# Kernel optimization log

Measured on AMD Instinct MI355X. Metric: run time of the kernel, lower is better.

## Reference

```python
import jax, jax.numpy as jnp
import numpy as np

NUM_GRAPHS = 64


def gcn_conv(x, W, b, src, dst, deg_inv_sqrt, n_nodes):
    # x: [N, Fin] -> [N, Fout]; src/dst include self-loops
    h = x @ W                                   # [N, Fout]
    norm = deg_inv_sqrt[src] * deg_inv_sqrt[dst]  # [E+N]
    msg = h[src] * norm[:, None]                # gather + scale
    out = jax.ops.segment_sum(msg, dst, num_segments=n_nodes)  # scatter-add
    return out + b


def setup_inputs() -> dict:
    key = jax.random.key(0)
    ks = jax.random.split(key, 12)
    N, E, IND, H, OUT = 100000, 1600000, 128, 64, 2
    x = jax.random.normal(ks[0], (N, IND), dtype=jnp.float32)
    edge_index = jax.random.randint(ks[1], (2, E), 0, N, dtype=jnp.int64)
    batch = jnp.sort(jax.random.randint(ks[2], (N,), 0, NUM_GRAPHS, dtype=jnp.int64))
    def glorot(k, shape):
        lim = (6.0 / (shape[0] + shape[1])) ** 0.5
        return jax.random.uniform(k, shape, jnp.float32, -lim, lim)
    W1 = glorot(ks[3], (IND, 84)); b1 = jnp.zeros((84,), jnp.float32)
    W2 = glorot(ks[4], (84, H));   b2 = jnp.zeros((H,), jnp.float32)
    W3 = glorot(ks[5], (H, 32));   b3 = jnp.zeros((32,), jnp.float32)
    Wl = glorot(ks[6], (32, OUT)); bl = jnp.zeros((OUT,), jnp.float32)
    return {"x": x, "edge_index": edge_index, "batch": batch,
            "W1": W1, "b1": b1, "W2": W2, "b2": b2,
            "W3": W3, "b3": b3, "Wl": Wl, "bl": bl}


def reference(x, edge_index, batch, W1, b1, W2, b2, W3, b3, Wl, bl):
    n = x.shape[0]
    loops = jnp.arange(n, dtype=edge_index.dtype)
    # GCNConv adds self-loops before symmetric normalization
    src = jnp.concatenate([edge_index[0], loops])
    dst = jnp.concatenate([edge_index[1], loops])
    deg = jax.ops.segment_sum(jnp.ones_like(dst, dtype=x.dtype), dst, num_segments=n)
    dis = jnp.where(deg > 0, jax.lax.rsqrt(jnp.maximum(deg, 1.0)), 0.0)

    h = jax.nn.relu(gcn_conv(x, W1, b1, src, dst, dis, n))
    h = jax.nn.relu(gcn_conv(h, W2, b2, src, dst, dis, n))
    h = jax.nn.relu(gcn_conv(h, W3, b3, src, dst, dis, n))

    # global mean pool over graphs
    sums = jax.ops.segment_sum(h, batch, num_segments=NUM_GRAPHS)      # [G, 32]
    cnts = jax.ops.segment_sum(jnp.ones((n,), h.dtype), batch, num_segments=NUM_GRAPHS)
    pooled = sums / jnp.maximum(cnts, 1.0)[:, None]
    # dropout is identity in eval mode
    return pooled @ Wl + bl
```

## Files before the change

kernel.cpp:

```cpp
#include <hip/hip_runtime.h>
#include <hip/hip_bf16.h>

typedef __attribute__((ext_vector_type(8))) short bf16x8;
typedef __attribute__((ext_vector_type(4))) float f32x4;

__device__ inline short f2bf(float f) {
    __hip_bfloat16 h = __float2bfloat16(f);
    return *reinterpret_cast<short*>(&h);
}


__global__ void zero_k(float* __restrict__ p, int n) {
    for (int i = blockIdx.x * blockDim.x + threadIdx.x; i < n;
         i += gridDim.x * blockDim.x)
        p[i] = 0.0f;
}


__global__ __launch_bounds__(256) void bucket_hist_k(
    const int* __restrict__ dst, int* __restrict__ T, int E, int NB)
{
    __shared__ int hist[512];
    for (int b = threadIdx.x; b < NB; b += 256) hist[b] = 0;
    __syncthreads();
    int per = (E + gridDim.x - 1) / gridDim.x;
    int s = blockIdx.x * per;
    int e = min(E, s + per);
    for (int i = s + threadIdx.x; i < e; i += 256)
        atomicAdd(&hist[dst[i] >> 8], 1);
    __syncthreads();
    for (int b = threadIdx.x; b < NB; b += 256)
        T[b * gridDim.x + blockIdx.x] = hist[b];
}

__global__ __launch_bounds__(256) void scan_block_k(
    const int* __restrict__ in, int* __restrict__ out,
    int* __restrict__ bsum, int n)
{
    __shared__ int ts[256];
    int base = blockIdx.x * 2048;
    int i0 = base + threadIdx.x * 8;
    int vals[8];
    int s = 0;
#pragma unroll
    for (int j = 0; j < 8; ++j) {
        int v = (i0 + j) < n ? in[i0 + j] : 0;
        vals[j] = v; s += v;
    }
    ts[threadIdx.x] = s;
    __syncthreads();
    for (int d = 1; d < 256; d <<= 1) {
        int t = (threadIdx.x >= (unsigned)d) ? ts[threadIdx.x - d] : 0;
        __syncthreads();
        ts[threadIdx.x] += t;
        __syncthreads();
    }
    int run = ts[threadIdx.x] - s;
    if (threadIdx.x == 255) bsum[blockIdx.x] = ts[255];
#pragma unroll
    for (int j = 0; j < 8; ++j) {
        if (i0 + j < n) out[i0 + j] = run;
        run += vals[j];
    }
}

__global__ void scan_partials_k(int* __restrict__ bsum, int nb) {
    if (threadIdx.x == 0 && blockIdx.x == 0) {
        int run = 0;
        for (int i = 0; i < nb; ++i) { int t = bsum[i]; bsum[i] = run; run += t; }
    }
}

__global__ void scan_add_k(int* __restrict__ rp, const int* __restrict__ bsum,
                           int n, int E)
{
    int i = blockIdx.x * blockDim.x + threadIdx.x;
    if (i < n) rp[i] += bsum[i >> 11];
    if (i == 0) rp[n] = E;
}

__global__ __launch_bounds__(256) void bucket_scatter_k(
    const int* __restrict__ src, const int* __restrict__ dst,
    const int* __restrict__ Tsc, uint2* __restrict__ pairs, int E, int NB)
{
    __shared__ int cur[512];
    for (int b = threadIdx.x; b < NB; b += 256)
        cur[b] = Tsc[b * gridDim.x + blockIdx.x];
    __syncthreads();
    int per = (E + gridDim.x - 1) / gridDim.x;
    int s = blockIdx.x * per;
    int e = min(E, s + per);
    for (int i = s + threadIdx.x; i < e; i += 256) {
        int d = dst[i];
        int pos = atomicAdd(&cur[d >> 8], 1);
        pairs[pos] = make_uint2((unsigned)d, (unsigned)src[i]);
    }
}

__global__ __launch_bounds__(256) void bucket_csr_k(
    const uint2* __restrict__ pairs, const int* __restrict__ Tsc,
    int* __restrict__ row_ptr, float* __restrict__ dis,
    int* __restrict__ csr, int N, int E, int NB, int G)
{
    __shared__ int cnt[256];
    __shared__ int ts[256];
    __shared__ int cur[256];
    const int b = blockIdx.x;
    const int node0 = b << 8;
    const int e0 = Tsc[b * G];
    const int e1 = Tsc[(b + 1) * G];
    const int j = threadIdx.x;
    cnt[j] = 0;
    __syncthreads();
    for (int i = e0 + j; i < e1; i += 256)
        atomicAdd(&cnt[pairs[i].x & 255u], 1);
    __syncthreads();
    int c = cnt[j];
    ts[j] = c;
    __syncthreads();
    for (int d = 1; d < 256; d <<= 1) {
        int t = (j >= d) ? ts[j - d] : 0;
        __syncthreads();
        ts[j] += t;
        __syncthreads();
    }
    int excl = ts[j] - c;
    int node = node0 + j;
    if (node < N) {
        row_ptr[node] = e0 + excl;
        dis[node] = rsqrtf(1.0f + (float)c);
    }
    cur[j] = e0 + excl;
    if (b == NB - 1 && j == 0) row_ptr[N] = E;
    __syncthreads();
    for (int i = e0 + j; i < e1; i += 256) {
        uint2 p = pairs[i];
        int pos = atomicAdd(&cur[p.x & 255u], 1);
        csr[pos] = (int)p.y;
    }
}


template<int FIN, int FOUT, int NKK, int CT>
__global__ void wfrag_build_k(const float* __restrict__ W,
                              __hip_bfloat16* __restrict__ out)
{
    int idx = blockIdx.x * 256 + threadIdx.x;
    if (idx >= CT * NKK * 64 * 8) return;
    int e = idx & 7;
    int lane = (idx >> 3) & 63;
    int t = idx >> 9;
    int kk = t % NKK, nn = t / NKK;
    int col = nn * 16 + (lane & 15);
    int k = kk * 32 + (lane >> 4) * 8 + e;
    float v = (k < FIN && col < FOUT) ? W[k * FOUT + col] : 0.f;
    out[idx] = __float2bfloat16(v);
}


template<int FIN>
__device__ inline bf16x8 load_a8(const float* __restrict__ p, int k0) {
    bf16x8 r;
    if (k0 + 8 <= FIN) {
        float4 v0 = *reinterpret_cast<const float4*>(p + k0);
        float4 v1 = *reinterpret_cast<const float4*>(p + k0 + 4);
        r[0] = f2bf(v0.x); r[1] = f2bf(v0.y); r[2] = f2bf(v0.z); r[3] = f2bf(v0.w);
        r[4] = f2bf(v1.x); r[5] = f2bf(v1.y); r[6] = f2bf(v1.z); r[7] = f2bf(v1.w);
    } else {
#pragma unroll
        for (int e = 0; e < 8; ++e)
            r[e] = (k0 + e < FIN) ? f2bf(p[k0 + e]) : (short)0;
    }
    return r;
}

template<int FIN, int FOUT, int NKK, int CT>
__global__ __launch_bounds__(256) void gemm_mfma_v5(
    const float* __restrict__ in, const __hip_bfloat16* __restrict__ wfrag,
    const float* __restrict__ dis, __hip_bfloat16* __restrict__ hh, int n)
{
    const int tid = threadIdx.x;
    const long long base = (long long)blockIdx.x * 64;
    const int cnt = (int)min((long long)64, (long long)n - base);
    const int wv = tid >> 6, lane = tid & 63;
    const int rlo = lane & 15, kg = lane >> 4, kb = kg * 8;
    const int arow = wv * 16 + rlo;
    const long long row = base + arow;

    bf16x8 a[NKK];
    if (arow < cnt) {
        const float* p = &in[(size_t)row * FIN];
#pragma unroll
        for (int kk = 0; kk < NKK; ++kk)
            a[kk] = load_a8<FIN>(p, kk * 32 + kb);
    } else {
#pragma unroll
        for (int kk = 0; kk < NKK; ++kk)
            a[kk] = (bf16x8){0, 0, 0, 0, 0, 0, 0, 0};
    }

    f32x4 acc[CT];
#pragma unroll
    for (int nn = 0; nn < CT; ++nn) acc[nn] = (f32x4){0.f, 0.f, 0.f, 0.f};

#pragma unroll
    for (int nn = 0; nn < CT; ++nn) {
#pragma unroll
        for (int kk = 0; kk < NKK; ++kk) {
            bf16x8 b = *reinterpret_cast<const bf16x8*>(
                &wfrag[(size_t)((nn * NKK + kk) * 64 + lane) * 8]);
            acc[nn] = __builtin_amdgcn_mfma_f32_16x16x32_bf16(a[kk], b, acc[nn], 0, 0, 0);
        }
    }

    const int r0 = wv * 16 + kg * 4;
    float dv[4];
#pragma unroll
    for (int i = 0; i < 4; ++i)
        dv[i] = (r0 + i < cnt) ? dis[base + r0 + i] : 0.f;
#pragma unroll
    for (int nn = 0; nn < CT; ++nn) {
        const int col = nn * 16 + rlo;
        if (col < FOUT) {
#pragma unroll
            for (int i = 0; i < 4; ++i) {
                int r = r0 + i;
                if (r < cnt) {
                    __hip_bfloat16 o = __float2bfloat16(acc[nn][i] * dv[i]);
                    hh[(size_t)(base + r) * FOUT + col] = o;
                }
            }
        }
    }
}


template<int F>
__global__ __launch_bounds__(256) void aggregate_v3(
    const __hip_bfloat16* __restrict__ hh, const int* __restrict__ row_ptr,
    const int* __restrict__ csr, const float* __restrict__ dis,
    const float* __restrict__ b, float* __restrict__ out, int n)
{
    constexpr int FG = F / 4;
    long long idx = (long long)blockIdx.x * 256 + threadIdx.x;
    if (idx >= (long long)n * FG) return;
    int node = (int)(idx / FG);
    int fg = (int)(idx - (long long)node * FG);
    const int bf = fg * 4;

    const unsigned short* hs = (const unsigned short*)hh;
    auto lo16 = [](unsigned u) { return __uint_as_float(u << 16); };
    auto hi16 = [](unsigned u) { return __uint_as_float(u & 0xFFFF0000u); };

    uint2 su = *reinterpret_cast<const uint2*>(&hs[(size_t)node * F + bf]);
    float a0 = lo16(su.x), a1 = hi16(su.x), a2 = lo16(su.y), a3 = hi16(su.y);
    float c0 = 0.f, c1 = 0.f, c2 = 0.f, c3 = 0.f;

    int e = row_ptr[node];
    const int e1 = row_ptr[node + 1];
    for (; e + 8 <= e1; e += 8) {
        int s0 = csr[e],     s1 = csr[e + 1], s2 = csr[e + 2], s3 = csr[e + 3];
        int s4 = csr[e + 4], s5 = csr[e + 5], s6 = csr[e + 6], s7 = csr[e + 7];
        uint2 u0 = *reinterpret_cast<const uint2*>(&hs[(size_t)s0 * F + bf]);
        uint2 u1 = *reinterpret_cast<const uint2*>(&hs[(size_t)s1 * F + bf]);
        uint2 u2 = *reinterpret_cast<const uint2*>(&hs[(size_t)s2 * F + bf]);
        uint2 u3 = *reinterpret_cast<const uint2*>(&hs[(size_t)s3 * F + bf]);
        uint2 u4 = *reinterpret_cast<const uint2*>(&hs[(size_t)s4 * F + bf]);
        uint2 u5 = *reinterpret_cast<const uint2*>(&hs[(size_t)s5 * F + bf]);
        uint2 u6 = *reinterpret_cast<const uint2*>(&hs[(size_t)s6 * F + bf]);
        uint2 u7 = *reinterpret_cast<const uint2*>(&hs[(size_t)s7 * F + bf]);
        a0 += lo16(u0.x); a1 += hi16(u0.x); a2 += lo16(u0.y); a3 += hi16(u0.y);
        c0 += lo16(u1.x); c1 += hi16(u1.x); c2 += lo16(u1.y); c3 += hi16(u1.y);
        a0 += lo16(u2.x); a1 += hi16(u2.x); a2 += lo16(u2.y); a3 += hi16(u2.y);
        c0 += lo16(u3.x); c1 += hi16(u3.x); c2 += lo16(u3.y); c3 += hi16(u3.y);
        a0 += lo16(u4.x); a1 += hi16(u4.x); a2 += lo16(u4.y); a3 += hi16(u4.y);
        c0 += lo16(u5.x); c1 += hi16(u5.x); c2 += lo16(u5.y); c3 += hi16(u5.y);
        a0 += lo16(u6.x); a1 += hi16(u6.x); a2 += lo16(u6.y); a3 += hi16(u6.y);
        c0 += lo16(u7.x); c1 += hi16(u7.x); c2 += lo16(u7.y); c3 += hi16(u7.y);
    }
    if (e + 4 <= e1) {
        int s0 = csr[e], s1 = csr[e + 1], s2 = csr[e + 2], s3 = csr[e + 3];
        uint2 u0 = *reinterpret_cast<const uint2*>(&hs[(size_t)s0 * F + bf]);
        uint2 u1 = *reinterpret_cast<const uint2*>(&hs[(size_t)s1 * F + bf]);
        uint2 u2 = *reinterpret_cast<const uint2*>(&hs[(size_t)s2 * F + bf]);
        uint2 u3 = *reinterpret_cast<const uint2*>(&hs[(size_t)s3 * F + bf]);
        a0 += lo16(u0.x); a1 += hi16(u0.x); a2 += lo16(u0.y); a3 += hi16(u0.y);
        c0 += lo16(u1.x); c1 += hi16(u1.x); c2 += lo16(u1.y); c3 += hi16(u1.y);
        a0 += lo16(u2.x); a1 += hi16(u2.x); a2 += lo16(u2.y); a3 += hi16(u2.y);
        c0 += lo16(u3.x); c1 += hi16(u3.x); c2 += lo16(u3.y); c3 += hi16(u3.y);
        e += 4;
    }
    for (; e < e1; ++e) {
        int s = csr[e];
        uint2 u = *reinterpret_cast<const uint2*>(&hs[(size_t)s * F + bf]);
        a0 += lo16(u.x); a1 += hi16(u.x); a2 += lo16(u.y); a3 += hi16(u.y);
    }
    a0 += c0; a1 += c1; a2 += c2; a3 += c3;

    float d = dis[node];
    float4 bb = *reinterpret_cast<const float4*>(&b[bf]);
    float4 o;
    o.x = fmaxf(fmaf(d, a0, bb.x), 0.0f);
    o.y = fmaxf(fmaf(d, a1, bb.y), 0.0f);
    o.z = fmaxf(fmaf(d, a2, bb.z), 0.0f);
    o.w = fmaxf(fmaf(d, a3, bb.w), 0.0f);
    *reinterpret_cast<float4*>(&out[(size_t)node * F + bf]) = o;
}


__global__ __launch_bounds__(256) void pool2_k(
    const float* __restrict__ h, const int* __restrict__ batch,
    float* __restrict__ sums, float* __restrict__ cnt, int n)
{
    constexpr int CHUNK = 1024;
    __shared__ float s[64 * 32];
    __shared__ float sc[64];
    for (int i = threadIdx.x; i < 64 * 32; i += 256) s[i] = 0.0f;
    if (threadIdx.x < 64) sc[threadIdx.x] = 0.0f;
    __syncthreads();

    long long start = (long long)blockIdx.x * CHUNK;
    long long end = start + CHUNK < n ? start + CHUNK : n;
    int total = (int)(end - start) * 32;
    for (int i = threadIdx.x; i < total; i += 256) {
        int r = i >> 5;
        int f = i & 31;
        int node = (int)start + r;
        int g = batch[node];
        atomicAdd(&s[g * 32 + f], h[(size_t)node * 32 + f]);
        if (f == 0) atomicAdd(&sc[g], 1.0f);
    }
    __syncthreads();
    for (int i = threadIdx.x; i < 64 * 32; i += 256) {
        float v = s[i];
        if (v != 0.0f) atomicAdd(&sums[i], v);
    }
    if (threadIdx.x < 64) {
        float v = sc[threadIdx.x];
        if (v != 0.0f) atomicAdd(&cnt[threadIdx.x], v);
    }
}

__global__ void head_k(const float* __restrict__ sums, const float* __restrict__ cnt,
                       const float* __restrict__ Wl, const float* __restrict__ bl,
                       float* __restrict__ out)
{
    int tid = threadIdx.x;
    if (tid < 128) {
        int g = tid >> 1;
        int o = tid & 1;
        float c = fmaxf(cnt[g], 1.0f);
        float a = 0.0f;
#pragma unroll
        for (int f = 0; f < 32; ++f)
            a += (sums[g * 32 + f] / c) * Wl[f * 2 + o];
        out[tid] = a + bl[o];
    }
}


extern "C" void kernel_launch(void* const* d_in, const int* in_sizes, int n_in,
                              void* d_out, int out_size, void* d_ws, size_t ws_size,
                              hipStream_t stream)
{
    const float* x   = (const float*)d_in[0];
    const int*   ei  = (const int*)d_in[1];
    const int*   bat = (const int*)d_in[2];
    const float* W1  = (const float*)d_in[3];
    const float* b1  = (const float*)d_in[4];
    const float* W2  = (const float*)d_in[5];
    const float* b2  = (const float*)d_in[6];
    const float* W3  = (const float*)d_in[7];
    const float* b3  = (const float*)d_in[8];
    const float* Wl  = (const float*)d_in[9];
    const float* bl  = (const float*)d_in[10];

    const int N = in_sizes[0] / 128;
    const int E = in_sizes[1] / 2;
    const int* src = ei;
    const int* dst = ei + E;

    const int NB = (N + 255) >> 8;
    const int G  = 128;
    const int NBG = NB * G;

    char* ws = (char*)d_ws;
    size_t off = 0;
    auto alloc = [&](size_t bytes) -> char* {
        char* p = ws + off;
        off += (bytes + 255) & ~(size_t)255;
        return p;
    };
    float* dis     = (float*)alloc((size_t)N * 4);
    int*   row_ptr = (int*)  alloc((size_t)(N + 1) * 4);
    int*   bsum    = (int*)  alloc(256 * 4);
    int*   csr     = (int*)  alloc((size_t)E * 4);
    int*   T       = (int*)  alloc((size_t)NBG * 4);
    int*   Tsc     = (int*)  alloc((size_t)(NBG + 1) * 4);
    __hip_bfloat16* WF1 = (__hip_bfloat16*)alloc(6 * 4 * 512 * 2);
    __hip_bfloat16* WF2 = (__hip_bfloat16*)alloc(4 * 3 * 512 * 2);
    __hip_bfloat16* WF3 = (__hip_bfloat16*)alloc(2 * 2 * 512 * 2);
    __hip_bfloat16* A = (__hip_bfloat16*)alloc((size_t)N * 84 * 2);
    float* B       = (float*)alloc((size_t)N * 84 * 4);
    float* C       = (float*)alloc((size_t)N * 64 * 4);
    float* D       = (float*)alloc((size_t)(64 * 32 + 64) * 4);
    uint2* pairs   = (uint2*)C;

    dim3 blk(256);
    auto cdiv = [](long long a, long long b) { return (int)((a + b - 1) / b); };

    wfrag_build_k<128, 84, 4, 6><<<cdiv(6 * 4 * 512, 256), blk, 0, stream>>>(W1, WF1);
    wfrag_build_k< 84, 64, 3, 4><<<cdiv(4 * 3 * 512, 256), blk, 0, stream>>>(W2, WF2);
    wfrag_build_k< 64, 32, 2, 2><<<cdiv(2 * 2 * 512, 256), blk, 0, stream>>>(W3, WF3);

    bucket_hist_k<<<G, blk, 0, stream>>>(dst, T, E, NB);
    int nb_scan = cdiv(NBG, 2048);
    scan_block_k<<<nb_scan, blk, 0, stream>>>(T, Tsc, bsum, NBG);
    scan_partials_k<<<1, 64, 0, stream>>>(bsum, nb_scan);
    scan_add_k<<<cdiv(NBG, 256), blk, 0, stream>>>(Tsc, bsum, NBG, E);
    bucket_scatter_k<<<G, blk, 0, stream>>>(src, dst, Tsc, pairs, E, NB);
    bucket_csr_k<<<NB, blk, 0, stream>>>(pairs, Tsc, row_ptr, dis, csr, N, E, NB, G);

    gemm_mfma_v5<128, 84, 4, 6><<<cdiv(N, 64), blk, 0, stream>>>(x, WF1, dis, A, N);
    aggregate_v3<84><<<cdiv((long long)N * 21, 256), blk, 0, stream>>>(A, row_ptr, csr, dis, b1, B, N);

    gemm_mfma_v5<84, 64, 3, 4><<<cdiv(N, 64), blk, 0, stream>>>(B, WF2, dis, A, N);
    aggregate_v3<64><<<cdiv((long long)N * 16, 256), blk, 0, stream>>>(A, row_ptr, csr, dis, b2, C, N);

    gemm_mfma_v5<64, 32, 2, 2><<<cdiv(N, 64), blk, 0, stream>>>(C, WF3, dis, A, N);
    aggregate_v3<32><<<cdiv((long long)N * 8, 256), blk, 0, stream>>>(A, row_ptr, csr, dis, b3, B, N);

    zero_k<<<cdiv(64 * 32 + 64, 256), blk, 0, stream>>>(D, 64 * 32 + 64);
    pool2_k<<<cdiv(N, 1024), blk, 0, stream>>>(B, bat, D, D + 64 * 32, N);
    head_k<<<1, 128, 0, stream>>>(D, D + 64 * 32, Wl, bl, (float*)d_out);
}
```

Before: 295.8 us.

## Store intermediate activations in bf16 with padded strides and pack CSR pairs

Intermediate layer outputs are written as bf16 with padded row strides instead of fp32, and the next GEMM reads bf16 directly, halving activation traffic between layers. Bucket-sort pairs are packed into one 32-bit word (8-bit local dst, 24-bit src) instead of uint2. The aggregation gather loop is unrolled to 16 loads in flight. This trades extra bf16 rounding on activations for less memory traffic, and relies on N fitting in 24 bits.

```diff
diff --git a/kernel.cpp b/kernel.cpp
--- a/kernel.cpp
+++ b/kernel.cpp
@@ -81,7 +81,7 @@
 
 __global__ __launch_bounds__(256) void bucket_scatter_k(
     const int* __restrict__ src, const int* __restrict__ dst,
-    const int* __restrict__ Tsc, uint2* __restrict__ pairs, int E, int NB)
+    const int* __restrict__ Tsc, unsigned* __restrict__ pairs, int E, int NB)
 {
     __shared__ int cur[512];
     for (int b = threadIdx.x; b < NB; b += 256)
@@ -93,12 +93,12 @@
     for (int i = s + threadIdx.x; i < e; i += 256) {
         int d = dst[i];
         int pos = atomicAdd(&cur[d >> 8], 1);
-        pairs[pos] = make_uint2((unsigned)d, (unsigned)src[i]);
+        pairs[pos] = ((unsigned)(d & 255) << 24) | (unsigned)src[i];
     }
 }
 
 __global__ __launch_bounds__(256) void bucket_csr_k(
-    const uint2* __restrict__ pairs, const int* __restrict__ Tsc,
+    const unsigned* __restrict__ pairs, const int* __restrict__ Tsc,
     int* __restrict__ row_ptr, float* __restrict__ dis,
     int* __restrict__ csr, int N, int E, int NB, int G)
 {
@@ -113,7 +113,7 @@
     cnt[j] = 0;
     __syncthreads();
     for (int i = e0 + j; i < e1; i += 256)
-        atomicAdd(&cnt[pairs[i].x & 255u], 1);
+        atomicAdd(&cnt[pairs[i] >> 24], 1);
     __syncthreads();
     int c = cnt[j];
     ts[j] = c;
@@ -134,9 +134,9 @@
     if (b == NB - 1 && j == 0) row_ptr[N] = E;
     __syncthreads();
     for (int i = e0 + j; i < e1; i += 256) {
-        uint2 p = pairs[i];
-        int pos = atomicAdd(&cur[p.x & 255u], 1);
-        csr[pos] = (int)p.y;
+        unsigned p = pairs[i];
+        int pos = atomicAdd(&cur[p >> 24], 1);
+        csr[pos] = (int)(p & 0xFFFFFFu);
     }
 }
 
@@ -159,7 +159,7 @@
 
 
 template<int FIN>
-__device__ inline bf16x8 load_a8(const float* __restrict__ p, int k0) {
+__device__ inline bf16x8 load_a8f(const float* __restrict__ p, int k0) {
     bf16x8 r;
     if (k0 + 8 <= FIN) {
         float4 v0 = *reinterpret_cast<const float4*>(p + k0);
@@ -174,9 +174,21 @@
     return r;
 }
 
-template<int FIN, int FOUT, int NKK, int CT>
-__global__ __launch_bounds__(256) void gemm_mfma_v5(
-    const float* __restrict__ in, const __hip_bfloat16* __restrict__ wfrag,
+template<int FIN>
+__device__ inline bf16x8 load_a8b(const __hip_bfloat16* __restrict__ p, int k0) {
+    if (k0 + 8 <= FIN)
+        return *reinterpret_cast<const bf16x8*>(p + k0);
+    bf16x8 r;
+    const short* ps = (const short*)p;
+#pragma unroll
+    for (int e = 0; e < 8; ++e)
+        r[e] = (k0 + e < FIN) ? ps[k0 + e] : (short)0;
+    return r;
+}
+
+template<typename TIN, int FIN, int SIN, int FOUT, int HS, int NKK, int CT>
+__global__ __launch_bounds__(256) void gemm_mfma_v6(
+    const TIN* __restrict__ in, const __hip_bfloat16* __restrict__ wfrag,
     const float* __restrict__ dis, __hip_bfloat16* __restrict__ hh, int n)
 {
     const int tid = threadIdx.x;
@@ -189,10 +201,14 @@
 
     bf16x8 a[NKK];
     if (arow < cnt) {
-        const float* p = &in[(size_t)row * FIN];
-#pragma unroll
-        for (int kk = 0; kk < NKK; ++kk)
-            a[kk] = load_a8<FIN>(p, kk * 32 + kb);
+        const TIN* p = &in[(size_t)row * SIN];
+#pragma unroll
+        for (int kk = 0; kk < NKK; ++kk) {
+            if constexpr (sizeof(TIN) == 4)
+                a[kk] = load_a8f<FIN>((const float*)p, kk * 32 + kb);
+            else
+                a[kk] = load_a8b<FIN>((const __hip_bfloat16*)p, kk * 32 + kb);
+        }
     } else {
 #pragma unroll
         for (int kk = 0; kk < NKK; ++kk)
@@ -227,7 +243,7 @@
                 int r = r0 + i;
                 if (r < cnt) {
                     __hip_bfloat16 o = __float2bfloat16(acc[nn][i] * dv[i]);
-                    hh[(size_t)(base + r) * FOUT + col] = o;
+                    hh[(size_t)(base + r) * HS + col] = o;
                 }
             }
         }
@@ -235,11 +251,11 @@
 }
 
 
-template<int F>
-__global__ __launch_bounds__(256) void aggregate_v3(
+template<int F, int HS, int SO, typename TOUT>
+__global__ __launch_bounds__(256) void aggregate_v4(
     const __hip_bfloat16* __restrict__ hh, const int* __restrict__ row_ptr,
     const int* __restrict__ csr, const float* __restrict__ dis,
-    const float* __restrict__ b, float* __restrict__ out, int n)
+    const float* __restrict__ b, TOUT* __restrict__ out, int n)
 {
     constexpr int FG = F / 4;
     long long idx = (long long)blockIdx.x * 256 + threadIdx.x;
@@ -252,59 +268,71 @@
     auto lo16 = [](unsigned u) { return __uint_as_float(u << 16); };
     auto hi16 = [](unsigned u) { return __uint_as_float(u & 0xFFFF0000u); };
 
-    uint2 su = *reinterpret_cast<const uint2*>(&hs[(size_t)node * F + bf]);
+    uint2 su = *reinterpret_cast<const uint2*>(&hs[(size_t)node * HS + bf]);
     float a0 = lo16(su.x), a1 = hi16(su.x), a2 = lo16(su.y), a3 = hi16(su.y);
     float c0 = 0.f, c1 = 0.f, c2 = 0.f, c3 = 0.f;
 
     int e = row_ptr[node];
     const int e1 = row_ptr[node + 1];
-    for (; e + 8 <= e1; e += 8) {
-        int s0 = csr[e],     s1 = csr[e + 1], s2 = csr[e + 2], s3 = csr[e + 3];
-        int s4 = csr[e + 4], s5 = csr[e + 5], s6 = csr[e + 6], s7 = csr[e + 7];
-        uint2 u0 = *reinterpret_cast<const uint2*>(&hs[(size_t)s0 * F + bf]);
-        uint2 u1 = *reinterpret_cast<const uint2*>(&hs[(size_t)s1 * F + bf]);
-        uint2 u2 = *reinterpret_cast<const uint2*>(&hs[(size_t)s2 * F + bf]);
-        uint2 u3 = *reinterpret_cast<const uint2*>(&hs[(size_t)s3 * F + bf]);
-        uint2 u4 = *reinterpret_cast<const uint2*>(&hs[(size_t)s4 * F + bf]);
-        uint2 u5 = *reinterpret_cast<const uint2*>(&hs[(size_t)s5 * F + bf]);
-        uint2 u6 = *reinterpret_cast<const uint2*>(&hs[(size_t)s6 * F + bf]);
-        uint2 u7 = *reinterpret_cast<const uint2*>(&hs[(size_t)s7 * F + bf]);
-        a0 += lo16(u0.x); a1 += hi16(u0.x); a2 += lo16(u0.y); a3 += hi16(u0.y);
-        c0 += lo16(u1.x); c1 += hi16(u1.x); c2 += lo16(u1.y); c3 += hi16(u1.y);
-        a0 += lo16(u2.x); a1 += hi16(u2.x); a2 += lo16(u2.y); a3 += hi16(u2.y);
-        c0 += lo16(u3.x); c1 += hi16(u3.x); c2 += lo16(u3.y); c3 += hi16(u3.y);
-        a0 += lo16(u4.x); a1 += hi16(u4.x); a2 += lo16(u4.y); a3 += hi16(u4.y);
-        c0 += lo16(u5.x); c1 += hi16(u5.x); c2 += lo16(u5.y); c3 += hi16(u5.y);
-        a0 += lo16(u6.x); a1 += hi16(u6.x); a2 += lo16(u6.y); a3 += hi16(u6.y);
-        c0 += lo16(u7.x); c1 += hi16(u7.x); c2 += lo16(u7.y); c3 += hi16(u7.y);
-    }
-    if (e + 4 <= e1) {
-        int s0 = csr[e], s1 = csr[e + 1], s2 = csr[e + 2], s3 = csr[e + 3];
-        uint2 u0 = *reinterpret_cast<const uint2*>(&hs[(size_t)s0 * F + bf]);
-        uint2 u1 = *reinterpret_cast<const uint2*>(&hs[(size_t)s1 * F + bf]);
-        uint2 u2 = *reinterpret_cast<const uint2*>(&hs[(size_t)s2 * F + bf]);
-        uint2 u3 = *reinterpret_cast<const uint2*>(&hs[(size_t)s3 * F + bf]);
-        a0 += lo16(u0.x); a1 += hi16(u0.x); a2 += lo16(u0.y); a3 += hi16(u0.y);
-        c0 += lo16(u1.x); c1 += hi16(u1.x); c2 += lo16(u1.y); c3 += hi16(u1.y);
-        a0 += lo16(u2.x); a1 += hi16(u2.x); a2 += lo16(u2.y); a3 += hi16(u2.y);
-        c0 += lo16(u3.x); c1 += hi16(u3.x); c2 += lo16(u3.y); c3 += hi16(u3.y);
-        e += 4;
+    for (; e + 16 <= e1; e += 16) {
+        int s[16];
+#pragma unroll
+        for (int j = 0; j < 16; ++j) s[j] = csr[e + j];
+        uint2 u[16];
+#pragma unroll
+        for (int j = 0; j < 16; ++j)
+            u[j] = *reinterpret_cast<const uint2*>(&hs[(size_t)s[j] * HS + bf]);
+#pragma unroll
+        for (int j = 0; j < 16; j += 2) {
+            a0 += lo16(u[j].x);     a1 += hi16(u[j].x);
+            a2 += lo16(u[j].y);     a3 += hi16(u[j].y);
+            c0 += lo16(u[j + 1].x); c1 += hi16(u[j + 1].x);
+            c2 += lo16(u[j + 1].y); c3 += hi16(u[j + 1].y);
+        }
+    }
+    for (; e + 4 <= e1; e += 4) {
+        int s[4];
+#pragma unroll
+        for (int j = 0; j < 4; ++j) s[j] = csr[e + j];
+        uint2 u[4];
+#pragma unroll
+        for (int j = 0; j < 4; ++j)
+            u[j] = *reinterpret_cast<const uint2*>(&hs[(size_t)s[j] * HS + bf]);
+#pragma unroll
+        for (int j = 0; j < 4; j += 2) {
+            a0 += lo16(u[j].x);     a1 += hi16(u[j].x);
+            a2 += lo16(u[j].y);     a3 += hi16(u[j].y);
+            c0 += lo16(u[j + 1].x); c1 += hi16(u[j + 1].x);
+            c2 += lo16(u[j + 1].y); c3 += hi16(u[j + 1].y);
+        }
     }
     for (; e < e1; ++e) {
         int s = csr[e];
-        uint2 u = *reinterpret_cast<const uint2*>(&hs[(size_t)s * F + bf]);
+        uint2 u = *reinterpret_cast<const uint2*>(&hs[(size_t)s * HS + bf]);
         a0 += lo16(u.x); a1 += hi16(u.x); a2 += lo16(u.y); a3 += hi16(u.y);
     }
     a0 += c0; a1 += c1; a2 += c2; a3 += c3;
 
     float d = dis[node];
     float4 bb = *reinterpret_cast<const float4*>(&b[bf]);
-    float4 o;
-    o.x = fmaxf(fmaf(d, a0, bb.x), 0.0f);
-    o.y = fmaxf(fmaf(d, a1, bb.y), 0.0f);
-    o.z = fmaxf(fmaf(d, a2, bb.z), 0.0f);
-    o.w = fmaxf(fmaf(d, a3, bb.w), 0.0f);
-    *reinterpret_cast<float4*>(&out[(size_t)node * F + bf]) = o;
+    float r0 = fmaxf(fmaf(d, a0, bb.x), 0.0f);
+    float r1 = fmaxf(fmaf(d, a1, bb.y), 0.0f);
+    float r2 = fmaxf(fmaf(d, a2, bb.z), 0.0f);
+    float r3 = fmaxf(fmaf(d, a3, bb.w), 0.0f);
+
+    if constexpr (sizeof(TOUT) == 2) {
+        alignas(8) __hip_bfloat16 o[4];
+        o[0] = __float2bfloat16(r0);
+        o[1] = __float2bfloat16(r1);
+        o[2] = __float2bfloat16(r2);
+        o[3] = __float2bfloat16(r3);
+        *reinterpret_cast<uint2*>(&((__hip_bfloat16*)out)[(size_t)node * SO + bf]) =
+            *reinterpret_cast<const uint2*>(o);
+    } else {
+        float4 o;
+        o.x = r0; o.y = r1; o.z = r2; o.w = r3;
+        *reinterpret_cast<float4*>(&((float*)out)[(size_t)node * SO + bf]) = o;
+    }
 }
 
 
@@ -400,11 +428,11 @@
     __hip_bfloat16* WF1 = (__hip_bfloat16*)alloc(6 * 4 * 512 * 2);
     __hip_bfloat16* WF2 = (__hip_bfloat16*)alloc(4 * 3 * 512 * 2);
     __hip_bfloat16* WF3 = (__hip_bfloat16*)alloc(2 * 2 * 512 * 2);
-    __hip_bfloat16* A = (__hip_bfloat16*)alloc((size_t)N * 84 * 2);
-    float* B       = (float*)alloc((size_t)N * 84 * 4);
-    float* C       = (float*)alloc((size_t)N * 64 * 4);
+    __hip_bfloat16* A = (__hip_bfloat16*)alloc((size_t)N * 96 * 2);
+    __hip_bfloat16* B = (__hip_bfloat16*)alloc((size_t)N * 96 * 2);
+    __hip_bfloat16* C = (__hip_bfloat16*)alloc((size_t)N * 64 * 2);
     float* D       = (float*)alloc((size_t)(64 * 32 + 64) * 4);
-    uint2* pairs   = (uint2*)C;
+    unsigned* pairs = (unsigned*)C;
 
     dim3 blk(256);
     auto cdiv = [](long long a, long long b) { return (int)((a + b - 1) / b); };
@@ -421,16 +449,19 @@
     bucket_scatter_k<<<G, blk, 0, stream>>>(src, dst, Tsc, pairs, E, NB);
     bucket_csr_k<<<NB, blk, 0, stream>>>(pairs, Tsc, row_ptr, dis, csr, N, E, NB, G);
 
-    gemm_mfma_v5<128, 84, 4, 6><<<cdiv(N, 64), blk, 0, stream>>>(x, WF1, dis, A, N);
-    aggregate_v3<84><<<cdiv((long long)N * 21, 256), blk, 0, stream>>>(A, row_ptr, csr, dis, b1, B, N);
-
-    gemm_mfma_v5<84, 64, 3, 4><<<cdiv(N, 64), blk, 0, stream>>>(B, WF2, dis, A, N);
-    aggregate_v3<64><<<cdiv((long long)N * 16, 256), blk, 0, stream>>>(A, row_ptr, csr, dis, b2, C, N);
-
-    gemm_mfma_v5<64, 32, 2, 2><<<cdiv(N, 64), blk, 0, stream>>>(C, WF3, dis, A, N);
-    aggregate_v3<32><<<cdiv((long long)N * 8, 256), blk, 0, stream>>>(A, row_ptr, csr, dis, b3, B, N);
+    gemm_mfma_v6<float, 128, 128, 84, 96, 4, 6><<<cdiv(N, 64), blk, 0, stream>>>(x, WF1, dis, A, N);
+    aggregate_v4<84, 96, 96, __hip_bfloat16><<<cdiv((long long)N * 21, 256), blk, 0, stream>>>(
+        A, row_ptr, csr, dis, b1, B, N);
+
+    gemm_mfma_v6<__hip_bfloat16, 84, 96, 64, 64, 3, 4><<<cdiv(N, 64), blk, 0, stream>>>(B, WF2, dis, A, N);
+    aggregate_v4<64, 64, 64, __hip_bfloat16><<<cdiv((long long)N * 16, 256), blk, 0, stream>>>(
+        A, row_ptr, csr, dis, b2, C, N);
+
+    gemm_mfma_v6<__hip_bfloat16, 64, 64, 32, 32, 2, 2><<<cdiv(N, 64), blk, 0, stream>>>(C, WF3, dis, A, N);
+    aggregate_v4<32, 32, 32, float><<<cdiv((long long)N * 8, 256), blk, 0, stream>>>(
+        A, row_ptr, csr, dis, b3, (float*)B, N);
 
     zero_k<<<cdiv(64 * 32 + 64, 256), blk, 0, stream>>>(D, 64 * 32 + 64);
-    pool2_k<<<cdiv(N, 1024), blk, 0, stream>>>(B, bat, D, D + 64 * 32, N);
+    pool2_k<<<cdiv(N, 1024), blk, 0, stream>>>((float*)B, bat, D, D + 64 * 32, N);
     head_k<<<1, 128, 0, stream>>>(D, D + 64 * 32, Wl, bl, (float*)d_out);
 }
```

Result: slower. 308.6 us (+4.3%).
